# Kernel optimization log

Hardware: AMD Instinct MI355X
Metric: run time of the kernel (lower is better)

## Reference

```python
import jax, jax.numpy as jnp
import numpy as np

NUM_HEADS = 8
DIM = 256
NW = 64  # number of windows per batch element


def setup_inputs() -> dict:
    key = jax.random.key(0)
    k_x, k_m, k_ws, k_wm, k_wp, k_bp = jax.random.split(key, 6)
    B_, N, C = 512, 128, DIM
    x = jax.random.normal(k_x, (B_, N, C), dtype=jnp.float32)
    # 0 / -100 additive attention mask (stand-in for the 0/-inf shift-window mask)
    mask = jnp.where(jax.random.uniform(k_m, (NW, N, N)) < 0.5, 0.0, -100.0).astype(jnp.float32)
    std = 0.02
    w_qkv_self = jax.random.normal(k_ws, (3 * C, C), dtype=jnp.float32) * std
    w_qkv_mut = jax.random.normal(k_wm, (3 * C, C), dtype=jnp.float32) * std
    w_proj = jax.random.normal(k_wp, (C, 2 * C), dtype=jnp.float32) * std
    b_proj = jax.random.normal(k_bp, (C,), dtype=jnp.float32) * std
    return {"x": x, "mask": mask, "w_qkv_self": w_qkv_self,
            "w_qkv_mut": w_qkv_mut, "w_proj": w_proj, "b_proj": b_proj}


def _split_qkv(x, w):
    # x: (B_, N, C); w: (3C, C) torch Linear weight -> y = x @ w.T
    B_, N, C = x.shape
    d = C // NUM_HEADS
    qkv = (x @ w.T).reshape(B_, N, 3, NUM_HEADS, d).transpose(2, 0, 3, 1, 4)
    return qkv[0], qkv[1], qkv[2]  # each (B_, H, N, d)


def _attention(q, k, v, mask, scale):
    # q,k,v: (B_, H, n, d); mask: (nW, Nfull, Nfull) additive
    B_, H, n, d = q.shape
    nW = mask.shape[0]
    attn = jnp.einsum('bhnd,bhmd->bhnm', q * scale, k)  # (B_, H, n, n)
    attn = attn.reshape(B_ // nW, nW, H, n, n) + mask[None, :, None, :n, :n]
    attn = jax.nn.softmax(attn.reshape(B_, H, n, n), axis=-1)
    out = jnp.einsum('bhnm,bhmd->bhnd', attn, v)
    return out.transpose(0, 2, 1, 3).reshape(B_, n, H * d)  # (B_, n, C)


def reference(x, mask, w_qkv_self, w_qkv_mut, w_proj, b_proj):
    B_, N, C = x.shape
    scale = (C // NUM_HEADS) ** (-0.5)
    # self window attention
    q, k, v = _split_qkv(x, w_qkv_self)
    x_out = _attention(q, k, v, mask, scale)  # (B_, N, C)
    # mutual (cross-frame) attention between the two halves of the window
    qm, km, vm = _split_qkv(x, w_qkv_mut)
    h = N // 2
    q1, q2 = qm[:, :, :h], qm[:, :, h:]
    k1, k2 = km[:, :, :h], km[:, :, h:]
    v1, v2 = vm[:, :, :h], vm[:, :, h:]
    x1_aligned = _attention(q2, k1, v1, mask, scale)  # (B_, N//2, C)
    x2_aligned = _attention(q1, k2, v2, mask, scale)  # (B_, N//2, C)
    x_mut = jnp.concatenate([x1_aligned, x2_aligned], axis=1)  # (B_, N, C)
    x_cat = jnp.concatenate([x_mut, x_out], axis=2)  # (B_, N, 2C)
    return x_cat @ w_proj.T + b_proj  # (B_, N, C)
```

## Files before the change

kernel.cpp:

```cpp
#include <hip/hip_runtime.h>
#include <stdint.h>

typedef __bf16 bf16x4 __attribute__((ext_vector_type(4)));
typedef __bf16 bf16x8 __attribute__((ext_vector_type(8)));
typedef float f32x4 __attribute__((ext_vector_type(4)));

#define DEVI __device__ __forceinline__

DEVI ushort bfbits(float f) {
  union { __bf16 b; ushort u; } v;
  v.b = (__bf16)f;
  return v.u;
}

DEVI void gload16(const void* g, void* l) {
  auto* gp = reinterpret_cast<const __attribute__((address_space(1))) uint32_t*>(
      reinterpret_cast<uintptr_t>(g));
  auto* lp = reinterpret_cast<__attribute__((address_space(3))) uint32_t*>(
      reinterpret_cast<uintptr_t>(l));
  __builtin_amdgcn_global_load_lds(gp, lp, 16, 0, 0);
}

__global__ __launch_bounds__(256) void cvt_x(const float* __restrict__ in,
                                             ushort* __restrict__ out) {
  int i = (blockIdx.x * 256 + threadIdx.x) * 4;
  float4 v = *(const float4*)(in + i);
  ushort4 o;
  o.x = bfbits(v.x); o.y = bfbits(v.y); o.z = bfbits(v.z); o.w = bfbits(v.w);
  *(ushort4*)(out + i) = o;
}

__global__ __launch_bounds__(256) void cvt_w(const float* __restrict__ ws,
                                             const float* __restrict__ wm,
                                             const float* __restrict__ wp,
                                             ushort* __restrict__ wqkv,
                                             ushort* __restrict__ wproj) {
  int i = blockIdx.x * 256 + threadIdx.x;
  if (i < 196608)       wqkv[i] = bfbits(ws[i]);
  else if (i < 393216)  wqkv[i] = bfbits(wm[i - 196608]);
  else                  wproj[i - 393216] = bfbits(wp[i - 393216]);
}

template <int KF, int NH>
DEVI void attn_body(const ushort* Qs, const ushort* Ks, const ushort* Vt,
                    ushort* Ps, const float* mrow, ushort* ob,
                    int qrow0, int kvbase, int orow0, int mrow0,
                    int lr, int lc) {
  const float L2E = 1.4426950408889634f;

  f32x4 sacc[2][KF];
#pragma unroll
  for (int mf = 0; mf < 2; ++mf)
#pragma unroll
    for (int nf = 0; nf < KF; ++nf) sacc[mf][nf] = (f32x4){0.f, 0.f, 0.f, 0.f};

  bf16x8 aq[2];
#pragma unroll
  for (int mf = 0; mf < 2; ++mf) {
    int r = qrow0 + mf * 16 + lr;
    aq[mf] = *(const bf16x8*)(Qs + r * 32 + ((lc ^ ((r >> 1) & 3)) * 8));
  }
  __builtin_amdgcn_s_setprio(1);
#pragma unroll
  for (int nf = 0; nf < KF; ++nf) {
    int r = kvbase + nf * 16 + lr;
    bf16x8 bk = *(const bf16x8*)(Ks + r * 32 + ((lc ^ ((r >> 1) & 3)) * 8));
#pragma unroll
    for (int mf = 0; mf < 2; ++mf)
      sacc[mf][nf] = __builtin_amdgcn_mfma_f32_16x16x32_bf16(aq[mf], bk, sacc[mf][nf], 0, 0, 0);
  }
  __builtin_amdgcn_s_setprio(0);

#pragma unroll
  for (int mf = 0; mf < 2; ++mf)
#pragma unroll
    for (int nf = 0; nf < KF; ++nf)
#pragma unroll
      for (int r = 0; r < 4; ++r) {
        int row = mrow0 + mf * 16 + lc * 4 + r;
        int col = nf * 16 + lr;
        sacc[mf][nf][r] = fmaf(mrow[row * 128 + col], L2E, sacc[mf][nf][r]);
      }
  float sinv[2][4];
#pragma unroll
  for (int mf = 0; mf < 2; ++mf)
#pragma unroll
    for (int r = 0; r < 4; ++r) {
      float s = 0.f;
#pragma unroll
      for (int nf = 0; nf < KF; ++nf) {
        float e = __builtin_amdgcn_exp2f(sacc[mf][nf][r]);
        sacc[mf][nf][r] = e;
        s += e;
      }
#pragma unroll
      for (int d = 1; d < 16; d <<= 1) s += __shfl_xor(s, d);
      sinv[mf][r] = __builtin_amdgcn_rcpf(s);
    }

  f32x4 oacc[2][2];
#pragma unroll
  for (int mf = 0; mf < 2; ++mf)
#pragma unroll
    for (int nf = 0; nf < 2; ++nf) oacc[mf][nf] = (f32x4){0.f, 0.f, 0.f, 0.f};

#pragma unroll
  for (int hf = 0; hf < NH; ++hf) {
    __syncthreads();
#pragma unroll
    for (int mf = 0; mf < 2; ++mf)
#pragma unroll
      for (int r = 0; r < 4; ++r) {
        int prow = orow0 + mf * 16 + lc * 4 + r;
#pragma unroll
        for (int nf2 = 0; nf2 < 4; ++nf2) {
          int col = nf2 * 16 + lr;
          int grp = (col >> 3) ^ (prow & 7);
          Ps[prow * 64 + grp * 8 + (col & 7)] = bfbits(sacc[mf][hf * 4 + nf2][r]);
        }
      }
    __syncthreads();
    __builtin_amdgcn_s_setprio(1);
#pragma unroll
    for (int ks = 0; ks < 2; ++ks) {
      bf16x8 pf[2], vf[2];
#pragma unroll
      for (int mf = 0; mf < 2; ++mf) {
        int prow = orow0 + mf * 16 + lr;
        int grp = (ks * 4 + lc) ^ (prow & 7);
        pf[mf] = *(const bf16x8*)(Ps + prow * 64 + grp * 8);
      }
#pragma unroll
      for (int nf = 0; nf < 2; ++nf)
        vf[nf] = *(const bf16x8*)(Vt + (nf * 16 + lr) * 136 + kvbase + hf * 64 + ks * 32 + lc * 8);
#pragma unroll
      for (int mf = 0; mf < 2; ++mf)
#pragma unroll
        for (int nf = 0; nf < 2; ++nf)
          oacc[mf][nf] = __builtin_amdgcn_mfma_f32_16x16x32_bf16(pf[mf], vf[nf], oacc[mf][nf], 0, 0, 0);
    }
    __builtin_amdgcn_s_setprio(0);
  }

#pragma unroll
  for (int mf = 0; mf < 2; ++mf)
#pragma unroll
    for (int nf = 0; nf < 2; ++nf)
#pragma unroll
      for (int r = 0; r < 4; ++r) {
        int row = orow0 + mf * 16 + lc * 4 + r;
        int col = nf * 16 + lr;
        ob[(size_t)row * 512 + col] = bfbits(oacc[mf][nf][r] * sinv[mf][r]);
      }
}

__global__ __launch_bounds__(256) void attn_fused(const ushort* __restrict__ xb,
                                                  const ushort* __restrict__ wqkv,
                                                  const float* __restrict__ mask,
                                                  ushort* __restrict__ xcat) {
  __shared__ __align__(16) uint8_t smem[39424];
  ushort* Qs = (ushort*)smem;
  ushort* Vt = (ushort*)(smem + 8192);
  uint8_t* REGION = smem + 16896;
  ushort* Ks = (ushort*)REGION;
  ushort* xs = (ushort*)(REGION + 8192);
  ushort* wl = (ushort*)(REGION + 16384);
  ushort* Ps = (ushort*)REGION;

  const int bid = blockIdx.x;
  const int c = bid & 7;
  const int u = bid >> 3;
  const int m = u & 1;
  const int h = (u >> 1) & 7;
  const int b = (u >> 4) * 8 + c;
  const int wmask = b & 63;
  const int t = threadIdx.x;
  const int wid = t >> 6, l = t & 63;
  const int lr = l & 15, lc = l >> 4;
  const float qscale = 0.17677669529663687f * 1.4426950408889634f;

  const ushort* xrow = xb + (size_t)b * 128 * 256;
  const int wbase = m * 768;

  f32x4 pacc[2][6];
#pragma unroll
  for (int mf = 0; mf < 2; ++mf)
#pragma unroll
    for (int n = 0; n < 6; ++n) pacc[mf][n] = (f32x4){0.f, 0.f, 0.f, 0.f};

  for (int kk = 0; kk < 256; kk += 32) {
    __syncthreads();
#pragma unroll
    for (int p = 0; p < 2; ++p) {
      int slot = t + p * 256;
      int row = slot >> 2, cs = slot & 3;
      int cd = cs ^ ((row >> 1) & 3);
      gload16(xrow + (size_t)row * 256 + kk + cd * 8, xs + slot * 8);
    }
    {
      int slot = t;
      int row = slot >> 2, cs = slot & 3;
      int cd = cs ^ ((row >> 1) & 3);
      int grow = wbase + (row >> 5) * 256 + h * 32 + (row & 31);
      gload16(wqkv + (size_t)grow * 256 + kk + cd * 8, wl + slot * 8);
    }
    if (t < 128) {
      int slot = t + 256;
      int row = slot >> 2, cs = slot & 3;
      int cd = cs ^ ((row >> 1) & 3);
      int grow = wbase + (row >> 5) * 256 + h * 32 + (row & 31);
      gload16(wqkv + (size_t)grow * 256 + kk + cd * 8, wl + slot * 8);
    }
    __syncthreads();

    bf16x8 ax[2];
#pragma unroll
    for (int mf = 0; mf < 2; ++mf) {
      int r = wid * 32 + mf * 16 + lr;
      ax[mf] = *(const bf16x8*)(xs + r * 32 + ((lc ^ ((r >> 1) & 3)) * 8));
    }
    __builtin_amdgcn_s_setprio(1);
#pragma unroll
    for (int n = 0; n < 6; ++n) {
      int r = n * 16 + lr;
      bf16x8 bw = *(const bf16x8*)(wl + r * 32 + ((lc ^ ((r >> 1) & 3)) * 8));
#pragma unroll
      for (int mf = 0; mf < 2; ++mf)
        pacc[mf][n] = __builtin_amdgcn_mfma_f32_16x16x32_bf16(ax[mf], bw, pacc[mf][n], 0, 0, 0);
    }
    __builtin_amdgcn_s_setprio(0);
  }

#pragma unroll
  for (int mf = 0; mf < 2; ++mf) {
#pragma unroll
    for (int n = 0; n < 4; ++n)
#pragma unroll
      for (int j = 0; j < 4; ++j) {
        int row = wid * 32 + mf * 16 + lc * 4 + j;
        int d = (n & 1) * 16 + lr;
        float v = pacc[mf][n][j];
        if (n < 2) v *= qscale;
        int sw = ((d >> 3) ^ ((row >> 1) & 3)) * 8 + (d & 7);
        (n < 2 ? Qs : Ks)[row * 32 + sw] = bfbits(v);
      }
#pragma unroll
    for (int k = 0; k < 2; ++k) {
      bf16x4 pk;
#pragma unroll
      for (int j = 0; j < 4; ++j) pk[j] = (__bf16)pacc[mf][4 + k][j];
      int d = k * 16 + lr;
      int row0 = wid * 32 + mf * 16 + lc * 4;
      *(bf16x4*)(Vt + d * 136 + row0) = pk;
    }
  }
  __syncthreads();

  const float* mrow = mask + (size_t)wmask * 16384;

  if (m == 0) {
    ushort* ob = xcat + (size_t)b * 128 * 512 + 256 + h * 32;
    attn_body<8, 2>(Qs, Ks, Vt, Ps, mrow, ob,
                    wid * 32, 0,
                    wid * 32, wid * 32, lr, lc);
  } else {
    const int half = wid >> 1, sub = wid & 1;
    ushort* ob = xcat + (size_t)b * 128 * 512 + h * 32;
    attn_body<4, 1>(Qs, Ks, Vt, Ps, mrow, ob,
                    (half ? 0 : 64) + sub * 32, half ? 64 : 0,
                    half * 64 + sub * 32, sub * 32, lr, lc);
  }
}

__global__ __launch_bounds__(256) void gemm_proj(const ushort* __restrict__ A,
                                                 const ushort* __restrict__ B,
                                                 const float* __restrict__ bias,
                                                 float* __restrict__ out) {
  __shared__ ushort As[128 * 32];
  __shared__ ushort Bs[256 * 32];
  const int t = threadIdx.x, tm = blockIdx.x;
  const int w = t >> 6, l = t & 63;
  const int wr = (w >> 1) * 64, wc = (w & 1) * 128;
  const int lr = l & 15, lc = l >> 4;
  const ushort* Ab = A + (size_t)tm * 128 * 512;

  f32x4 acc[4][8];
#pragma unroll
  for (int m = 0; m < 4; ++m)
#pragma unroll
    for (int n = 0; n < 8; ++n) acc[m][n] = (f32x4){0.f, 0.f, 0.f, 0.f};

  for (int kk = 0; kk < 512; kk += 32) {
    __syncthreads();
#pragma unroll
    for (int p = 0; p < 2; ++p) {
      int slot = t + p * 256;
      int row = slot >> 2, cs = slot & 3;
      int cd = cs ^ ((row >> 1) & 3);
      gload16(Ab + (size_t)row * 512 + kk + cd * 8, As + slot * 8);
    }
#pragma unroll
    for (int p = 0; p < 4; ++p) {
      int slot = t + p * 256;
      int row = slot >> 2, cs = slot & 3;
      int cd = cs ^ ((row >> 1) & 3);
      gload16(B + (size_t)row * 512 + kk + cd * 8, Bs + slot * 8);
    }
    __syncthreads();

    bf16x8 af[4], bfr[8];
#pragma unroll
    for (int m = 0; m < 4; ++m) {
      int r = wr + m * 16 + lr;
      af[m] = *(const bf16x8*)(As + r * 32 + ((lc ^ ((r >> 1) & 3)) * 8));
    }
#pragma unroll
    for (int n = 0; n < 8; ++n) {
      int r = wc + n * 16 + lr;
      bfr[n] = *(const bf16x8*)(Bs + r * 32 + ((lc ^ ((r >> 1) & 3)) * 8));
    }
#pragma unroll
    for (int m = 0; m < 4; ++m)
#pragma unroll
      for (int n = 0; n < 8; ++n)
        acc[m][n] = __builtin_amdgcn_mfma_f32_16x16x32_bf16(af[m], bfr[n], acc[m][n], 0, 0, 0);
  }

#pragma unroll
  for (int m = 0; m < 4; ++m)
#pragma unroll
    for (int n = 0; n < 8; ++n)
#pragma unroll
      for (int r = 0; r < 4; ++r) {
        int row = tm * 128 + wr + m * 16 + lc * 4 + r;
        int col = wc + n * 16 + lr;
        out[(size_t)row * 256 + col] = acc[m][n][r] + bias[col];
      }
}

extern "C" void kernel_launch(void* const* d_in, const int* in_sizes, int n_in,
                              void* d_out, int out_size, void* d_ws, size_t ws_size,
                              hipStream_t stream) {
  const float* x = (const float*)d_in[0];
  const float* mask = (const float*)d_in[1];
  const float* w_qkv_self = (const float*)d_in[2];
  const float* w_qkv_mut = (const float*)d_in[3];
  const float* w_proj = (const float*)d_in[4];
  const float* b_proj = (const float*)d_in[5];
  float* out = (float*)d_out;

  uint8_t* ws = (uint8_t*)d_ws;
  ushort* xb    = (ushort*)(ws);
  ushort* wqkv  = (ushort*)(ws + 33554432);
  ushort* wproj = (ushort*)(ws + 34340864);
  ushort* xcat  = (ushort*)d_out;

  cvt_x<<<dim3(16384), dim3(256), 0, stream>>>(x, xb);
  cvt_w<<<dim3(2048), dim3(256), 0, stream>>>(w_qkv_self, w_qkv_mut, w_proj, wqkv, wproj);
  attn_fused<<<dim3(8192), dim3(256), 0, stream>>>(xb, wqkv, mask, xcat);
  gemm_proj<<<dim3(512), dim3(256), 0, stream>>>(xcat, wproj, b_proj, out);
}
```

Baseline: 187.5 us.

## Load QKV x operand directly to registers, double K-step, shrink LDS for occupancy

The QKV projection loop in the fused attention kernel now reads each wave's x rows straight from global memory into registers instead of staging them through LDS. The K step grows from 32 to 64, which halves the number of barriers, and the weight tile uses a new 8-way XOR swizzle. The LDS layout is repacked into a smaller footprint and launch bounds now request 4 blocks per CU to raise occupancy. In exchange there are more in-flight register loads and tighter register limits, which could cause spills.

```diff
diff --git a/kernel.cpp b/kernel.cpp
--- a/kernel.cpp
+++ b/kernel.cpp
@@ -154,18 +154,16 @@
       }
 }
 
-__global__ __launch_bounds__(256) void attn_fused(const ushort* __restrict__ xb,
-                                                  const ushort* __restrict__ wqkv,
-                                                  const float* __restrict__ mask,
-                                                  ushort* __restrict__ xcat) {
-  __shared__ __align__(16) uint8_t smem[39424];
+__global__ __launch_bounds__(256, 4) void attn_fused(const ushort* __restrict__ xb,
+                                                     const ushort* __restrict__ wqkv,
+                                                     const float* __restrict__ mask,
+                                                     ushort* __restrict__ xcat) {
+  __shared__ __align__(16) uint8_t smem[37376];
   ushort* Qs = (ushort*)smem;
-  ushort* Vt = (ushort*)(smem + 8192);
-  uint8_t* REGION = smem + 16896;
-  ushort* Ks = (ushort*)REGION;
-  ushort* xs = (ushort*)(REGION + 8192);
-  ushort* wl = (ushort*)(REGION + 16384);
-  ushort* Ps = (ushort*)REGION;
+  ushort* Ks = (ushort*)(smem + 8192);
+  ushort* Vt = (ushort*)(smem + 16384);
+  ushort* wl = (ushort*)(smem + 25088);
+  ushort* Ps = (ushort*)smem;
 
   const int bid = blockIdx.x;
   const int c = bid & 7;
@@ -179,8 +177,8 @@
   const int lr = l & 15, lc = l >> 4;
   const float qscale = 0.17677669529663687f * 1.4426950408889634f;
 
-  const ushort* xrow = xb + (size_t)b * 128 * 256;
   const int wbase = m * 768;
+  const ushort* xp = xb + (size_t)b * 128 * 256 + (size_t)(wid * 32 + lr) * 256 + lc * 8;
 
   f32x4 pacc[2][6];
 #pragma unroll
@@ -188,46 +186,36 @@
 #pragma unroll
     for (int n = 0; n < 6; ++n) pacc[mf][n] = (f32x4){0.f, 0.f, 0.f, 0.f};
 
-  for (int kk = 0; kk < 256; kk += 32) {
-    __syncthreads();
-#pragma unroll
-    for (int p = 0; p < 2; ++p) {
+  for (int kk = 0; kk < 256; kk += 64) {
+    __syncthreads();
+#pragma unroll
+    for (int p = 0; p < 3; ++p) {
       int slot = t + p * 256;
-      int row = slot >> 2, cs = slot & 3;
-      int cd = cs ^ ((row >> 1) & 3);
-      gload16(xrow + (size_t)row * 256 + kk + cd * 8, xs + slot * 8);
-    }
-    {
-      int slot = t;
-      int row = slot >> 2, cs = slot & 3;
-      int cd = cs ^ ((row >> 1) & 3);
+      int row = slot >> 3, cs = slot & 7;
+      int cd = cs ^ (row & 7);
       int grow = wbase + (row >> 5) * 256 + h * 32 + (row & 31);
       gload16(wqkv + (size_t)grow * 256 + kk + cd * 8, wl + slot * 8);
     }
-    if (t < 128) {
-      int slot = t + 256;
-      int row = slot >> 2, cs = slot & 3;
-      int cd = cs ^ ((row >> 1) & 3);
-      int grow = wbase + (row >> 5) * 256 + h * 32 + (row & 31);
-      gload16(wqkv + (size_t)grow * 256 + kk + cd * 8, wl + slot * 8);
-    }
-    __syncthreads();
-
-    bf16x8 ax[2];
-#pragma unroll
-    for (int mf = 0; mf < 2; ++mf) {
-      int r = wid * 32 + mf * 16 + lr;
-      ax[mf] = *(const bf16x8*)(xs + r * 32 + ((lc ^ ((r >> 1) & 3)) * 8));
-    }
+    bf16x8 ax[2][2];
+#pragma unroll
+    for (int mf = 0; mf < 2; ++mf)
+#pragma unroll
+      for (int k2 = 0; k2 < 2; ++k2)
+        ax[mf][k2] = *(const bf16x8*)(xp + mf * 4096 + kk + k2 * 32);
+    __syncthreads();
+
     __builtin_amdgcn_s_setprio(1);
 #pragma unroll
-    for (int n = 0; n < 6; ++n) {
-      int r = n * 16 + lr;
-      bf16x8 bw = *(const bf16x8*)(wl + r * 32 + ((lc ^ ((r >> 1) & 3)) * 8));
-#pragma unroll
-      for (int mf = 0; mf < 2; ++mf)
-        pacc[mf][n] = __builtin_amdgcn_mfma_f32_16x16x32_bf16(ax[mf], bw, pacc[mf][n], 0, 0, 0);
-    }
+    for (int k2 = 0; k2 < 2; ++k2)
+#pragma unroll
+      for (int n = 0; n < 6; ++n) {
+        int r = n * 16 + lr;
+        int g = (k2 * 4 + lc) ^ (r & 7);
+        bf16x8 bw = *(const bf16x8*)(wl + r * 64 + g * 8);
+#pragma unroll
+        for (int mf = 0; mf < 2; ++mf)
+          pacc[mf][n] = __builtin_amdgcn_mfma_f32_16x16x32_bf16(ax[mf][k2], bw, pacc[mf][n], 0, 0, 0);
+      }
     __builtin_amdgcn_s_setprio(0);
   }
 
```

Measured after the change: 233.3 us. 24.4% more time.
